# Kernel optimization log

Measured on AMD Instinct MI355X. Metric: run time of the kernel, lower is better.

## Reference

```python
import jax, jax.numpy as jnp
import numpy as np

HEADS = 8
HID = 128
N_A = 10000
N_B = 10000
E = 120000
NG = 8  # graphs in batch
F_A = 256
F_B = 128
NEG_SLOPE = 0.2


def _gat(h_src, h_dst, src, dst, ws, wd, a_s, a_d, bias, num_dst):
    """PyG GATConv, bipartite, concat=False, add_self_loops=False."""
    hs = (h_src @ ws).reshape(-1, HEADS, HID)   # [N_src, H, C]
    hd = (h_dst @ wd).reshape(-1, HEADS, HID)   # [N_dst, H, C]
    al_s = jnp.sum(hs * a_s, axis=-1)           # [N_src, H]
    al_d = jnp.sum(hd * a_d, axis=-1)           # [N_dst, H]
    e = jax.nn.leaky_relu(al_s[src] + al_d[dst], NEG_SLOPE)  # [E, H]
    m = jax.ops.segment_max(e, dst, num_segments=num_dst)
    ex = jnp.exp(e - m[dst])
    denom = jax.ops.segment_sum(ex, dst, num_segments=num_dst)
    alpha = ex / (denom[dst] + 1e-16)           # segment softmax over in-edges
    msg = hs[src] * alpha[:, :, None]           # [E, H, C]
    out = jax.ops.segment_sum(msg, dst, num_segments=num_dst)
    return out.mean(axis=1) + bias              # concat=False -> head mean + bias


def _mean_pool(x, batch, num_graphs):
    s = jax.ops.segment_sum(x, batch, num_segments=num_graphs)
    cnt = jax.ops.segment_sum(jnp.ones((x.shape[0],), x.dtype), batch, num_segments=num_graphs)
    return s / jnp.maximum(cnt, 1.0)[:, None]


def setup_inputs() -> dict:
    key = jax.random.key(0)
    ks = iter(jax.random.split(key, 48))
    rn = lambda shape, s=0.05: jax.random.normal(next(ks), shape, jnp.float32) * s
    inp = {
        'x_a': jax.random.normal(next(ks), (N_A, F_A), jnp.float32),
        'x_b': jax.random.normal(next(ks), (N_B, F_B), jnp.float32),
        'edge_ab': jax.random.randint(next(ks), (2, E), 0, N_A, jnp.int32),
        'edge_ba': jax.random.randint(next(ks), (2, E), 0, N_B, jnp.int32),
        'batch_a': jnp.sort(jax.random.randint(next(ks), (N_A,), 0, NG, jnp.int32)),
        'batch_b': jnp.sort(jax.random.randint(next(ks), (N_B,), 0, NG, jnp.int32)),
        'lin_a_w': rn((F_A, HID)), 'lin_a_b': rn((HID,)),
        'lin_b_w': rn((F_B, HID)), 'lin_b_b': rn((HID,)),
        'fc_w': rn((2 * HID, 1)), 'fc_b': rn((1,)),
    }
    for layer in ('1', '2'):
        for rel in ('ab', 'ba'):
            inp[f'w{layer}s_{rel}'] = rn((HID, HEADS * HID))
            inp[f'w{layer}d_{rel}'] = rn((HID, HEADS * HID))
            inp[f'a{layer}s_{rel}'] = rn((HEADS, HID))
            inp[f'a{layer}d_{rel}'] = rn((HEADS, HID))
            inp[f'b{layer}_{rel}'] = rn((HID,))
    return inp


def reference(x_a, x_b, edge_ab, edge_ba, batch_a, batch_b,
              lin_a_w, lin_a_b, lin_b_w, lin_b_b, fc_w, fc_b,
              w1s_ab, w1d_ab, a1s_ab, a1d_ab, b1_ab,
              w1s_ba, w1d_ba, a1s_ba, a1d_ba, b1_ba,
              w2s_ab, w2d_ab, a2s_ab, a2d_ab, b2_ab,
              w2s_ba, w2d_ba, a2s_ba, a2d_ba, b2_ba):
    ha = jax.nn.relu(x_a @ lin_a_w + lin_a_b)
    hb = jax.nn.relu(x_b @ lin_b_w + lin_b_b)
    # layer 1 (each dst type receives exactly one relation -> HeteroConv mean is identity)
    hb1 = _gat(ha, hb, edge_ab[0], edge_ab[1], w1s_ab, w1d_ab, a1s_ab, a1d_ab, b1_ab, N_B)
    ha1 = _gat(hb, ha, edge_ba[0], edge_ba[1], w1s_ba, w1d_ba, a1s_ba, a1d_ba, b1_ba, N_A)
    ha1 = jax.nn.relu(ha1)
    hb1 = jax.nn.relu(hb1)
    # layer 2
    hb2 = _gat(ha1, hb1, edge_ab[0], edge_ab[1], w2s_ab, w2d_ab, a2s_ab, a2d_ab, b2_ab, N_B)
    ha2 = _gat(hb1, ha1, edge_ba[0], edge_ba[1], w2s_ba, w2d_ba, a2s_ba, a2d_ba, b2_ba, N_A)
    pa = _mean_pool(ha2, batch_a, NG)
    pb = _mean_pool(hb2, batch_b, NG)
    g = jnp.concatenate([pa, pb], axis=1)       # [NG, 2*HID]
    return (g @ fc_w + fc_b).squeeze(-1)        # [NG]
```

## Files before the change

kernel.cpp:

```cpp
#include <hip/hip_runtime.h>
#include <math.h>

#define HID 128
#define HEADS 8

typedef __attribute__((ext_vector_type(8))) short s16x8;
typedef __attribute__((ext_vector_type(4))) float f32x4;

__device__ __forceinline__ unsigned short bf16_rne(float x) {
  unsigned u = __float_as_uint(x);
  unsigned r = u + 0x7FFFu + ((u >> 16) & 1u);
  return (unsigned short)(r >> 16);
}
__device__ __forceinline__ float bf16f(unsigned short h) {
  return __uint_as_float(((unsigned)h) << 16);
}

struct RSeg { float* out; const float* bias; int M; int rowbase; };

__global__ __launch_bounds__(256) void reduce_epi(
    const float* __restrict__ P, int Mtot, int KS, float scale, int do_relu,
    RSeg s0, RSeg s1)
{
  int idx = blockIdx.x * 256 + threadIdx.x;
  if (idx >= Mtot * 32) return;
  int r = idx >> 5;
  int c = (idx & 31) << 2;
  float* outp; const float* bias; int rl;
  if (s1.M > 0 && r >= s1.rowbase) {
    rl = r - s1.rowbase; if (rl >= s1.M) return; outp = s1.out; bias = s1.bias;
  } else {
    rl = r; if (rl >= s0.M) return; outp = s0.out; bias = s0.bias;
  }
  float4 acc = make_float4(0.f, 0.f, 0.f, 0.f);
  for (int z = 0; z < KS; z++) {
    const float4 v = *(const float4*)(P + ((size_t)z * Mtot + r) * HID + c);
    acc.x += v.x; acc.y += v.y; acc.z += v.z; acc.w += v.w;
  }
  const float4 b = *(const float4*)(bias + c);
  acc.x = acc.x * scale + b.x;
  acc.y = acc.y * scale + b.y;
  acc.z = acc.z * scale + b.z;
  acc.w = acc.w * scale + b.w;
  if (do_relu) {
    acc.x = acc.x > 0.f ? acc.x : 0.f;
    acc.y = acc.y > 0.f ? acc.y : 0.f;
    acc.z = acc.z > 0.f ? acc.z : 0.f;
    acc.w = acc.w > 0.f ? acc.w : 0.f;
  }
  *(float4*)(outp + (size_t)rl * HID + c) = acc;
}

struct PrepArgs {
  const float* W[8];
  const float* a[8];
  unsigned short* WThi[4];
  unsigned short* WTlo[4];
  float* v[8];
};

__global__ __launch_bounds__(256) void prep_hist(
    PrepArgs p, const int* __restrict__ dst_ab, const int* __restrict__ dst_ba,
    int* __restrict__ cnt_ab, int* __restrict__ cnt_ba, int E)
{
  int bid = blockIdx.x;
  if (bid < 2048) {
    int g = bid >> 9;
    int idx = ((bid & 511) << 8) + threadIdx.x;
    int kidx = idx & 1023;
    int c = idx >> 10;
    int h = kidx >> 7, k = kidx & 127;
    float wv = p.W[2 * g][(size_t)k * (HEADS * HID) + h * HID + c];
    unsigned short hi = bf16_rne(wv);
    unsigned short lo = bf16_rne(wv - bf16f(hi));
    p.WThi[g][idx] = hi;
    p.WTlo[g][idx] = lo;
  } else if (bid < 2080) {
    int u = bid - 2048;
    int wi = u >> 2;
    int gid = ((u & 3) << 8) + threadIdx.x;
    int k = gid >> 3, h = gid & 7;
    const float* wr = p.W[wi] + (size_t)k * (HEADS * HID) + h * HID;
    const float* ar = p.a[wi] + (size_t)h * HID;
    float s = 0.f;
    for (int c = 0; c < HID; c++) s = fmaf(wr[c], ar[c], s);
    p.v[wi][gid] = s;
  } else {
    int gid = (bid - 2080) * 256 + threadIdx.x;
    if (gid < E) atomicAdd(&cnt_ab[dst_ab[gid]], 1);
    else if (gid < 2 * E) atomicAdd(&cnt_ba[dst_ba[gid - E]], 1);
  }
}

__global__ __launch_bounds__(1024) void scan2(
    const int* __restrict__ cnt_ab, const int* __restrict__ cnt_ba,
    int* __restrict__ ip_ab, int* __restrict__ ip_ba, int n_ab, int n_ba)
{
  const int* cnt = (blockIdx.x == 0) ? cnt_ab : cnt_ba;
  int* indptr = (blockIdx.x == 0) ? ip_ab : ip_ba;
  int n = (blockIdx.x == 0) ? n_ab : n_ba;
  __shared__ int parts[1024];
  const int tid = threadIdx.x;
  const int base = tid * 10;
  int local[10];
  int s = 0;
#pragma unroll
  for (int j = 0; j < 10; j++) {
    int v = (base + j < n) ? cnt[base + j] : 0;
    local[j] = v; s += v;
  }
  parts[tid] = s;
  __syncthreads();
  for (int off = 1; off < 1024; off <<= 1) {
    int v = (tid >= off) ? parts[tid - off] : 0;
    __syncthreads();
    parts[tid] += v;
    __syncthreads();
  }
  int ex = parts[tid] - s;
#pragma unroll
  for (int j = 0; j < 10; j++) {
    if (base + j < n) indptr[base + j] = ex;
    ex += local[j];
  }
  if (tid == 1023) indptr[n] = parts[1023];
}

struct GSeg { const float* A; const float* B; int M; int K; int yb; };

__global__ __launch_bounds__(256, 3) void scatter_gemm_in(
    const int* __restrict__ edge_ab, const int* __restrict__ edge_ba,
    const int* __restrict__ ip_ab, const int* __restrict__ ip_ba,
    int* __restrict__ cur_ab, int* __restrict__ cur_ba,
    int* __restrict__ srcs_ab, int* __restrict__ srcs_ba, int E, int scat_b,
    GSeg s0, GSeg s1, float* __restrict__ P, int Mtot, int KS)
{
  __shared__ float As[16][132];
  __shared__ float Bs[16][132];
  const int bid0 = blockIdx.x;
  if (bid0 < scat_b) {
    int gid = bid0 * 256 + threadIdx.x;
    if (gid < E) {
      int d = edge_ab[E + gid];
      int pos = ip_ab[d] + atomicAdd(&cur_ab[d], 1);
      srcs_ab[pos] = edge_ab[gid];
    } else if (gid < 2 * E) {
      int g = gid - E;
      int d = edge_ba[E + g];
      int pos = ip_ba[d] + atomicAdd(&cur_ba[d], 1);
      srcs_ba[pos] = edge_ba[g];
    }
    return;
  }
  const int gg = bid0 - scat_b;
  const int nxt = s0.yb + s1.yb;
  const int bx = gg % nxt;
  const int by = gg / nxt;

  const int tid = threadIdx.x;
  const float* A; const float* B; int M, K, rowbase, ytile;
  if (bx < s0.yb) {
    A = s0.A; B = s0.B; M = s0.M; K = s0.K; rowbase = 0; ytile = bx;
  } else {
    A = s1.A; B = s1.B; M = s1.M; K = s1.K; rowbase = s0.yb * 128; ytile = bx - s0.yb;
  }
  const int bm = ytile * 128;
  const int kchunk = K / KS;
  const int kbeg = by * kchunk;

  const int am = tid >> 1;
  const int ak = (tid & 1) << 3;
  const int brr = tid >> 4;
  const int bcc = (tid & 15) << 2;
  const int tx = tid & 15, ty = tid >> 4;

  float acc[64];
#pragma unroll
  for (int i = 0; i < 64; i++) acc[i] = 0.f;

  const int gr = bm + am;
  const float* Arow = A + (size_t)gr * K;
  for (int k0 = kbeg; k0 < kbeg + kchunk; k0 += 16) {
    float4 av0 = make_float4(0.f, 0.f, 0.f, 0.f), av1 = av0;
    if (gr < M) {
      av0 = *(const float4*)(Arow + k0 + ak);
      av1 = *(const float4*)(Arow + k0 + ak + 4);
    }
    const float4 bv0 = *(const float4*)(B + (size_t)(k0 + brr) * HID + bcc);
    const float4 bv1 = *(const float4*)(B + (size_t)(k0 + brr) * HID + bcc + 64);
    As[ak + 0][am] = av0.x; As[ak + 1][am] = av0.y;
    As[ak + 2][am] = av0.z; As[ak + 3][am] = av0.w;
    As[ak + 4][am] = av1.x; As[ak + 5][am] = av1.y;
    As[ak + 6][am] = av1.z; As[ak + 7][am] = av1.w;
    *(float4*)&Bs[brr][bcc] = bv0;
    *(float4*)&Bs[brr][bcc + 64] = bv1;
    __syncthreads();
#pragma unroll
    for (int kk = 0; kk < 16; kk++) {
      const float4 a0 = *(const float4*)&As[kk][ty << 3];
      const float4 a1 = *(const float4*)&As[kk][(ty << 3) + 4];
      const float4 b0 = *(const float4*)&Bs[kk][tx << 3];
      const float4 b1 = *(const float4*)&Bs[kk][(tx << 3) + 4];
      const float ar[8] = {a0.x, a0.y, a0.z, a0.w, a1.x, a1.y, a1.z, a1.w};
      const float bq[8] = {b0.x, b0.y, b0.z, b0.w, b1.x, b1.y, b1.z, b1.w};
#pragma unroll
      for (int i = 0; i < 8; i++)
#pragma unroll
        for (int j = 0; j < 8; j++) acc[i * 8 + j] = fmaf(ar[i], bq[j], acc[i * 8 + j]);
    }
    __syncthreads();
  }
  const size_t prow0 = (size_t)by * Mtot + rowbase + bm;
#pragma unroll
  for (int i = 0; i < 8; i++) {
    float* pp = P + (prow0 + (ty << 3) + i) * HID + (tx << 3);
    *(float4*)pp       = make_float4(acc[i * 8 + 0], acc[i * 8 + 1], acc[i * 8 + 2], acc[i * 8 + 3]);
    *(float4*)(pp + 4) = make_float4(acc[i * 8 + 4], acc[i * 8 + 5], acc[i * 8 + 6], acc[i * 8 + 7]);
  }
}

__global__ __launch_bounds__(256) void compute_al4(
    const float* __restrict__ ha, const float* __restrict__ hb,
    const float* __restrict__ v4,
    float* __restrict__ o0, float* __restrict__ o1,
    float* __restrict__ o2, float* __restrict__ o3, int na, int nb)
{
  __shared__ float vsh[4 * HID * HEADS];
  for (int i = threadIdx.x; i < 4 * HID * HEADS; i += 256) vsh[i] = v4[i];
  __syncthreads();
  int gid = blockIdx.x * 256 + threadIdx.x;
  int row = gid >> 3, h = gid & 7;
  const float* hr; float* o; int q, rl;
  if (row < na)                    { q = 0; rl = row;               hr = ha; o = o0; }
  else if (row < na + nb)          { q = 1; rl = row - na;          hr = hb; o = o1; }
  else if (row < na + 2 * nb)      { q = 2; rl = row - na - nb;     hr = hb; o = o2; }
  else if (row < 2 * na + 2 * nb)  { q = 3; rl = row - na - 2 * nb; hr = ha; o = o3; }
  else return;
  hr += (size_t)rl * HID;
  const float* vq = vsh + q * HID * HEADS;
  float s = 0.f;
  for (int k = 0; k < HID; k++) s = fmaf(hr[k], vq[k * HEADS + h], s);
  o[(size_t)rl * HEADS + h] = s;
}

struct GDir {
  const int* indptr; const int* srcs;
  const float* als; const float* ald;
  const float* h;
  unsigned short* zhi; unsigned short* zlo;
};

__global__ __launch_bounds__(256) void gat_edge2(GDir d0, GDir d1, int n0, int ntot)
{
  const int w = threadIdx.x >> 6;
  const int lane = threadIdx.x & 63;
  const int g = blockIdx.x * 4 + w;
  if (g >= ntot) return;
  const bool first = (g < n0);
  const int n = first ? g : g - n0;
  const int* indptr = first ? d0.indptr : d1.indptr;
  const int* srcs   = first ? d0.srcs   : d1.srcs;
  const float* als  = first ? d0.als    : d1.als;
  const float* ald  = first ? d0.ald    : d1.ald;
  const float* hsrc = first ? d0.h      : d1.h;
  unsigned short* zh = (first ? d0.zhi : d1.zhi) + (size_t)n * (HEADS * HID);
  unsigned short* zl = (first ? d0.zlo : d1.zlo) + (size_t)n * (HEADS * HID);

  const int base = indptr[n];
  const int deg = indptr[n + 1] - base;
  if (deg == 0) {
#pragma unroll
    for (int hh = 0; hh < HEADS; hh++) {
      *(unsigned*)(zh + hh * HID + 2 * lane) = 0u;
      *(unsigned*)(zl + hh * HID + 2 * lane) = 0u;
    }
    return;
  }
  const int eh = lane >> 3, h = lane & 7;
  const float aldn = ald[(size_t)n * HEADS + h];
  const int nch = (deg + 7) >> 3;
  const int ncc = nch < 4 ? nch : 4;

  int sc[4];
  float vc[4];
#pragma unroll
  for (int c = 0; c < 4; c++) {
    int e = c * 8 + eh;
    sc[c] = (c < ncc && e < deg) ? srcs[base + e] : -1;
  }
#pragma unroll
  for (int c = 0; c < 4; c++)
    vc[c] = (sc[c] >= 0) ? als[(size_t)sc[c] * HEADS + h] : 0.f;
  float den = 0.f;
#pragma unroll
  for (int c = 0; c < 4; c++) {
    float v = vc[c] + aldn;
    v = v > 0.f ? v : 0.2f * v;
    float ex = (sc[c] >= 0) ? expf(v) : 0.f;
    vc[c] = ex;
    den += ex;
  }
  for (int e0 = 32; e0 < deg; e0 += 8) {
    int e = e0 + eh;
    if (e < deg) {
      int s = srcs[base + e];
      float v = als[(size_t)s * HEADS + h] + aldn;
      v = v > 0.f ? v : 0.2f * v;
      den += expf(v);
    }
  }
  den += __shfl_xor(den, 8);
  den += __shfl_xor(den, 16);
  den += __shfl_xor(den, 32);

  float acc[16];
#pragma unroll
  for (int i = 0; i < 16; i++) acc[i] = 0.f;
#pragma unroll
  for (int c = 0; c < 4; c++) {
    if (c >= ncc) break;
    const int rem = deg - c * 8;
    const int elim = rem < 8 ? rem : 8;
#pragma unroll
    for (int half = 0; half < 2; half++) {
      if (half * 4 >= elim) break;
      int sj[4];
#pragma unroll
      for (int j = 0; j < 4; j++) {
        int s = __shfl(sc[c], (half * 4 + j) * 8);
        sj[j] = s < 0 ? 0 : s;
      }
      float2 hv[4];
#pragma unroll
      for (int j = 0; j < 4; j++)
        hv[j] = *(const float2*)(hsrc + (size_t)sj[j] * HID + 2 * lane);
#pragma unroll
      for (int j = 0; j < 4; j++) {
#pragma unroll
        for (int hh = 0; hh < 8; hh++) {
          float a = __shfl(vc[c], (half * 4 + j) * 8 + hh);
          acc[2 * hh]     = fmaf(a, hv[j].x, acc[2 * hh]);
          acc[2 * hh + 1] = fmaf(a, hv[j].y, acc[2 * hh + 1]);
        }
      }
    }
  }
  for (int e0 = 32; e0 < deg; e0 += 8) {
    int e = e0 + eh;
    int s = (e < deg) ? srcs[base + e] : -1;
    float ex = 0.f;
    if (s >= 0) {
      float v = als[(size_t)s * HEADS + h] + aldn;
      v = v > 0.f ? v : 0.2f * v;
      ex = expf(v);
    }
    int elim = deg - e0; if (elim > 8) elim = 8;
    for (int e8 = 0; e8 < elim; e8++) {
      int ss = __shfl(s, e8 * 8);
      const float2 hvt = *(const float2*)(hsrc + (size_t)ss * HID + 2 * lane);
#pragma unroll
      for (int hh = 0; hh < 8; hh++) {
        float a = __shfl(ex, e8 * 8 + hh);
        acc[2 * hh]     = fmaf(a, hvt.x, acc[2 * hh]);
        acc[2 * hh + 1] = fmaf(a, hvt.y, acc[2 * hh + 1]);
      }
    }
  }
#pragma unroll
  for (int hh = 0; hh < 8; hh++) {
    float dh = __shfl(den, hh);
    float inv = 1.f / (dh + 1e-16f);
    float x0 = acc[2 * hh] * inv;
    float x1 = acc[2 * hh + 1] * inv;
    unsigned short h0 = bf16_rne(x0), h1 = bf16_rne(x1);
    unsigned short l0 = bf16_rne(x0 - bf16f(h0)), l1 = bf16_rne(x1 - bf16f(h1));
    *(unsigned*)(zh + hh * HID + 2 * lane) = (unsigned)h0 | ((unsigned)h1 << 16);
    *(unsigned*)(zl + hh * HID + 2 * lane) = (unsigned)l0 | ((unsigned)l1 << 16);
  }
}

struct MSeg {
  const unsigned short* Ahi; const unsigned short* Alo;
  const unsigned short* Bhi; const unsigned short* Blo;
  float* out; const float* bias; int M; int yb;
};

__global__ __launch_bounds__(512) void gemm_mfma8(MSeg s0, MSeg s1, float scale, int do_relu)
{
  __shared__ __align__(16) unsigned short smem[24576];
  const int tid = threadIdx.x;
  const unsigned short *Ahi, *Alo, *Bhi, *Blo; const float* bias; float* out; int M, ytile;
  if ((int)blockIdx.x < s0.yb) {
    Ahi = s0.Ahi; Alo = s0.Alo; Bhi = s0.Bhi; Blo = s0.Blo;
    out = s0.out; bias = s0.bias; M = s0.M; ytile = blockIdx.x;
  } else {
    Ahi = s1.Ahi; Alo = s1.Alo; Bhi = s1.Bhi; Blo = s1.Blo;
    out = s1.out; bias = s1.bias; M = s1.M; ytile = blockIdx.x - s0.yb;
  }
  const int bm = ytile * 64;
  const int half = tid >> 8;
  const int t = tid & 255;
  const int kbase = half * 512;
  unsigned short* sm = smem + half * 12288;

  const int sr = t >> 2;
  const int sg = t & 3;
  const int g1 = sg ^ ((sr >> 1) & 3);
  const int sr2 = sr + 64;
  const int g2 = sg ^ ((sr2 >> 1) & 3);
  const int aslot  = sr * 32 + g1 * 8;
  const int bslotA = sr * 32 + g1 * 8;
  const int bslotB = sr2 * 32 + g2 * 8;
  const unsigned short* gA  = Ahi + (size_t)(bm + sr) * 1024 + kbase + sg * 8;
  const unsigned short* gAl = Alo + (size_t)(bm + sr) * 1024 + kbase + sg * 8;
  const unsigned short* gB0 = Bhi + (size_t)sr  * 1024 + kbase + sg * 8;
  const unsigned short* gB1 = Bhi + (size_t)sr2 * 1024 + kbase + sg * 8;
  const unsigned short* gC0 = Blo + (size_t)sr  * 1024 + kbase + sg * 8;
  const unsigned short* gC1 = Blo + (size_t)sr2 * 1024 + kbase + sg * 8;

  const int l = t & 63;
  const int w = t >> 6;
  const int kg = l >> 4;
  int aoff[4], boff[2];
#pragma unroll
  for (int mi = 0; mi < 4; mi++) {
    int r = mi * 16 + (l & 15);
    aoff[mi] = r * 32 + (kg ^ ((r >> 1) & 3)) * 8;
  }
#pragma unroll
  for (int ni = 0; ni < 2; ni++) {
    int r = w * 32 + ni * 16 + (l & 15);
    boff[ni] = r * 32 + (kg ^ ((r >> 1) & 3)) * 8;
  }

  f32x4 acc[4][2];
  const f32x4 z4 = {0.f, 0.f, 0.f, 0.f};
#pragma unroll
  for (int mi = 0; mi < 4; mi++)
#pragma unroll
    for (int ni = 0; ni < 2; ni++) acc[mi][ni] = z4;

  uint4 rA  = *(const uint4*)gA;
  uint4 rAl = *(const uint4*)gAl;
  uint4 rB0 = *(const uint4*)gB0;
  uint4 rB1 = *(const uint4*)gB1;
  uint4 rC0 = *(const uint4*)gC0;
  uint4 rC1 = *(const uint4*)gC1;

  for (int ks = 0; ks < 16; ks++) {
    *(uint4*)&sm[aslot]         = rA;
    *(uint4*)&sm[2048 + aslot]  = rAl;
    *(uint4*)&sm[4096 + bslotA] = rB0;
    *(uint4*)&sm[4096 + bslotB] = rB1;
    *(uint4*)&sm[8192 + bslotA] = rC0;
    *(uint4*)&sm[8192 + bslotB] = rC1;
    __syncthreads();
    if (ks < 15) {
      const int k0 = (ks + 1) * 32;
      rA  = *(const uint4*)(gA  + k0);
      rAl = *(const uint4*)(gAl + k0);
      rB0 = *(const uint4*)(gB0 + k0);
      rB1 = *(const uint4*)(gB1 + k0);
      rC0 = *(const uint4*)(gC0 + k0);
      rC1 = *(const uint4*)(gC1 + k0);
    }
    s16x8 bh0 = *(const s16x8*)&sm[4096 + boff[0]];
    s16x8 bh1 = *(const s16x8*)&sm[4096 + boff[1]];
    s16x8 bl0 = *(const s16x8*)&sm[8192 + boff[0]];
    s16x8 bl1 = *(const s16x8*)&sm[8192 + boff[1]];
#pragma unroll
    for (int mi = 0; mi < 4; mi++) {
      s16x8 ah = *(const s16x8*)&sm[aoff[mi]];
      s16x8 al = *(const s16x8*)&sm[2048 + aoff[mi]];
      acc[mi][0] = __builtin_amdgcn_mfma_f32_16x16x32_bf16(ah, bh0, acc[mi][0], 0, 0, 0);
      acc[mi][1] = __builtin_amdgcn_mfma_f32_16x16x32_bf16(ah, bh1, acc[mi][1], 0, 0, 0);
      acc[mi][0] = __builtin_amdgcn_mfma_f32_16x16x32_bf16(ah, bl0, acc[mi][0], 0, 0, 0);
      acc[mi][1] = __builtin_amdgcn_mfma_f32_16x16x32_bf16(ah, bl1, acc[mi][1], 0, 0, 0);
      acc[mi][0] = __builtin_amdgcn_mfma_f32_16x16x32_bf16(al, bh0, acc[mi][0], 0, 0, 0);
      acc[mi][1] = __builtin_amdgcn_mfma_f32_16x16x32_bf16(al, bh1, acc[mi][1], 0, 0, 0);
      acc[mi][0] = __builtin_amdgcn_mfma_f32_16x16x32_bf16(al, bl0, acc[mi][0], 0, 0, 0);
      acc[mi][1] = __builtin_amdgcn_mfma_f32_16x16x32_bf16(al, bl1, acc[mi][1], 0, 0, 0);
    }
    __syncthreads();
  }

  float* fred = (float*)smem;
  const int q = l >> 4, cl = l & 15;
  if (half == 1) {
#pragma unroll
    for (int ni = 0; ni < 2; ni++) {
      const int col = w * 32 + ni * 16 + cl;
#pragma unroll
      for (int mi = 0; mi < 4; mi++) {
        const f32x4 v = acc[mi][ni];
#pragma unroll
        for (int j = 0; j < 4; j++)
          fred[(mi * 16 + q * 4 + j) * 128 + col] = v[j];
      }
    }
  }
  __syncthreads();
  if (half == 0) {
#pragma unroll
    for (int ni = 0; ni < 2; ni++) {
      const int col = w * 32 + ni * 16 + cl;
      const float bv = bias[col];
#pragma unroll
      for (int mi = 0; mi < 4; mi++) {
        const int rt = mi * 16 + q * 4;
        const f32x4 v = acc[mi][ni];
#pragma unroll
        for (int j = 0; j < 4; j++) {
          const int r = bm + rt + j;
          if (r < M) {
            float x = (v[j] + fred[(rt + j) * 128 + col]) * scale + bv;
            if (do_relu) x = fmaxf(x, 0.f);
            out[(size_t)r * HID + col] = x;
          }
        }
      }
    }
  }
}

__global__ __launch_bounds__(256) void pool_fin(
    const float* __restrict__ ha, const float* __restrict__ hb,
    const int* __restrict__ batch_a, const int* __restrict__ batch_b,
    const float* __restrict__ fc_w, const float* __restrict__ fc_b,
    float* __restrict__ gsum, int* __restrict__ ticket,
    float* __restrict__ out, int na, int nb, int ng)
{
  const bool isA = blockIdx.x < 160;
  const float* h = isA ? ha : hb;
  const int* batch = isA ? batch_a : batch_b;
  const float* wseg = isA ? fc_w : fc_w + HID;
  float* gs = isA ? gsum : gsum + 8;
  const int n = isA ? na : nb;
  const int b = isA ? blockIdx.x : blockIdx.x - 160;

  __shared__ float sg[8];
  __shared__ int lastf;
  if (threadIdx.x < 8) sg[threadIdx.x] = 0.f;
  __syncthreads();
  const int lane = threadIdx.x & 63;
  const int wv = threadIdx.x >> 6;
  const int gw = b * 4 + wv;
  const int tw = 160 * 4;
  const float2 w2 = *(const float2*)(wseg + lane * 2);
  for (int r = gw; r < n; r += tw) {
    float2 hv = *(const float2*)(h + (size_t)r * HID + lane * 2);
    float s = hv.x * w2.x + hv.y * w2.y;
#pragma unroll
    for (int off = 32; off > 0; off >>= 1) s += __shfl_down(s, off, 64);
    if (lane == 0) atomicAdd(&sg[batch[r]], s);
  }
  __syncthreads();
  if (threadIdx.x < 8) atomicAdd(&gs[threadIdx.x], sg[threadIdx.x]);
  if (threadIdx.x == 0) {
    __threadfence();
    int tk = atomicAdd(ticket, 1);
    lastf = (tk == (int)gridDim.x - 1);
  }
  __syncthreads();
  if (lastf) {
    int g = threadIdx.x;
    if (g < ng) {
      int l, r, lo;
      l = 0; r = na; while (l < r) { int m = (l + r) >> 1; if (batch_a[m] < g) l = m + 1; else r = m; } lo = l;
      r = na; while (l < r) { int m = (l + r) >> 1; if (batch_a[m] < g + 1) l = m + 1; else r = m; }
      int ca = l - lo; if (ca < 1) ca = 1;
      l = 0; r = nb; while (l < r) { int m = (l + r) >> 1; if (batch_b[m] < g) l = m + 1; else r = m; } lo = l;
      r = nb; while (l < r) { int m = (l + r) >> 1; if (batch_b[m] < g + 1) l = m + 1; else r = m; }
      int cb = l - lo; if (cb < 1) cb = 1;
      float va = atomicAdd(&gsum[g], 0.f);
      float vb = atomicAdd(&gsum[8 + g], 0.f);
      out[g] = va / (float)ca + vb / (float)cb + fc_b[0];
    }
  }
}

extern "C" void kernel_launch(void* const* d_in, const int* in_sizes, int n_in,
                              void* d_out, int out_size, void* d_ws, size_t ws_size,
                              hipStream_t stream)
{
  const float* x_a = (const float*)d_in[0];
  const float* x_b = (const float*)d_in[1];
  const int* edge_ab = (const int*)d_in[2];
  const int* edge_ba = (const int*)d_in[3];
  const int* batch_a = (const int*)d_in[4];
  const int* batch_b = (const int*)d_in[5];
  const float* lin_a_w = (const float*)d_in[6];
  const float* lin_a_b = (const float*)d_in[7];
  const float* lin_b_w = (const float*)d_in[8];
  const float* lin_b_b = (const float*)d_in[9];
  const float* fc_w = (const float*)d_in[10];
  const float* fc_b = (const float*)d_in[11];

  const int NA = in_sizes[4];
  const int NB = in_sizes[5];
  const int E  = in_sizes[2] / 2;
  const int FA = in_sizes[0] / NA;
  const int FB = in_sizes[1] / NB;
  const int NG = out_size;
  const int NMAX = NA > NB ? NA : NB;
  const int NAp = (NA + 127) & ~127, NBp = (NB + 127) & ~127;
  const int NMAXp = NAp > NBp ? NAp : NBp;
  const int yba = NAp / 128, ybb = NBp / 128;
  const int Mtot = NAp + NBp;

  auto al256 = [](size_t b) { return (b + 255) & ~(size_t)255; };
  size_t fixed = 0;
  fixed += 3 * al256((size_t)NAp * HID * 4) + 3 * al256((size_t)NBp * HID * 4);
  fixed += 2 * al256((size_t)NMAXp * 1024 * 2);
  fixed += al256((size_t)8 * 131072 * 2);
  fixed += al256((size_t)8 * HID * HEADS * 4);
  fixed += 2 * al256((size_t)NAp * HEADS * 4) + 2 * al256((size_t)NBp * HEADS * 4);
  fixed += al256(((size_t)4 * NMAX + 24) * 4);
  fixed += al256((size_t)(NB + 1) * 4) + al256((size_t)(NA + 1) * 4);
  fixed += 2 * al256((size_t)E * 4);
  fixed += 8192;
  const size_t zba_sz = 2 * al256((size_t)NAp * 1024 * 2);
  const size_t pslice = al256((size_t)Mtot * HID * 4);

  int KS = 4; bool dual = true;
  if (fixed + zba_sz + 4 * pslice <= ws_size)      { dual = true;  KS = 4; }
  else if (fixed + zba_sz + 2 * pslice <= ws_size) { dual = true;  KS = 2; }
  else if (fixed + 4 * pslice <= ws_size)          { dual = false; KS = 4; }
  else if (fixed + 2 * pslice <= ws_size)          { dual = false; KS = 2; }
  else if (fixed + 1 * pslice <= ws_size)          { dual = false; KS = 1; }
  else return;

  char* w = (char*)d_ws;
  auto carve = [&](size_t bytes) -> void* {
    void* p = (void*)w;
    w += (bytes + 255) & ~(size_t)255;
    return p;
  };
  float* ha0 = (float*)carve((size_t)NAp * HID * 4);
  float* hb0 = (float*)carve((size_t)NBp * HID * 4);
  float* ha1 = (float*)carve((size_t)NAp * HID * 4);
  float* hb1 = (float*)carve((size_t)NBp * HID * 4);
  float* ha2 = (float*)carve((size_t)NAp * HID * 4);
  float* hb2 = (float*)carve((size_t)NBp * HID * 4);
  unsigned short* zab_hi = (unsigned short*)carve((size_t)NMAXp * 1024 * 2);
  unsigned short* zab_lo = (unsigned short*)carve((size_t)NMAXp * 1024 * 2);
  unsigned short* zba_hi = dual ? (unsigned short*)carve((size_t)NAp * 1024 * 2) : zab_hi;
  unsigned short* zba_lo = dual ? (unsigned short*)carve((size_t)NAp * 1024 * 2) : zab_lo;
  float* P   = (float*)carve((size_t)KS * Mtot * HID * 4);
  unsigned short* WT = (unsigned short*)carve((size_t)8 * 131072 * 2);
  float* vv  = (float*)carve((size_t)8 * HID * HEADS * 4);
  float* als_ab = (float*)carve((size_t)NAp * HEADS * 4);
  float* ald_ab = (float*)carve((size_t)NBp * HEADS * 4);
  float* als_ba = (float*)carve((size_t)NBp * HEADS * 4);
  float* ald_ba = (float*)carve((size_t)NAp * HEADS * 4);
  int* csrblk = (int*)carve(((size_t)4 * NMAX + 24) * 4);
  int* indptr_ab = (int*)carve((size_t)(NB + 1) * 4);
  int* indptr_ba = (int*)carve((size_t)(NA + 1) * 4);
  int* srcs_ab   = (int*)carve((size_t)E * 4);
  int* srcs_ba   = (int*)carve((size_t)E * 4);
  if ((size_t)(w - (char*)d_ws) > ws_size) return;

  int* cnt_ab = csrblk;
  int* cnt_ba = csrblk + NMAX;
  int* cur_ab = csrblk + 2 * NMAX;
  int* cur_ba = csrblk + 3 * NMAX;
  float* gsum = (float*)(csrblk + 4 * NMAX);
  int* ticket = csrblk + 4 * NMAX + 16;

  hipMemsetAsync(csrblk, 0, ((size_t)4 * NMAX + 24) * 4, stream);

  PrepArgs pa;
  const int wi_idx[8] = {12, 13, 17, 18, 22, 23, 27, 28};
  const int ai_idx[8] = {14, 15, 19, 20, 24, 25, 29, 30};
  for (int i = 0; i < 8; i++) {
    pa.W[i] = (const float*)d_in[wi_idx[i]];
    pa.a[i] = (const float*)d_in[ai_idx[i]];
    pa.v[i] = vv + (size_t)i * HID * HEADS;
  }
  for (int g = 0; g < 4; g++) {
    pa.WThi[g] = WT + (size_t)g * 131072;
    pa.WTlo[g] = WT + (size_t)(4 + g) * 131072;
  }
  const int hist_b = (2 * E + 255) / 256;
  prep_hist<<<2080 + hist_b, 256, 0, stream>>>(pa, edge_ab + E, edge_ba + E,
                                               cnt_ab, cnt_ba, E);
  scan2<<<2, 1024, 0, stream>>>(cnt_ab, cnt_ba, indptr_ab, indptr_ba, NB, NA);

  {
    GSeg sa = {x_a, lin_a_w, NA, FA, yba};
    GSeg sb = {x_b, lin_b_w, NB, FB, ybb};
    const int scat_b = (2 * E + 255) / 256;
    scatter_gemm_in<<<scat_b + (yba + ybb) * KS, 256, 0, stream>>>(
        edge_ab, edge_ba, indptr_ab, indptr_ba, cur_ab, cur_ba,
        srcs_ab, srcs_ba, E, scat_b, sa, sb, P, Mtot, KS);
    RSeg ra = {ha0, lin_a_b, NA, 0};
    RSeg rb = {hb0, lin_b_b, NB, yba * 128};
    reduce_epi<<<(Mtot * 32 + 255) / 256, 256, 0, stream>>>(P, Mtot, KS, 1.f, 1, ra, rb);
  }

  auto run_layer = [&](int L, const float* haP, const float* hbP,
                       float* haN, float* hbN, const float* b_ab, const float* b_ba,
                       int relu) {
    compute_al4<<<((2 * (NA + NB)) * HEADS + 255) / 256, 256, 0, stream>>>(
        haP, hbP, vv + (size_t)L * 4 * HID * HEADS,
        als_ab, ald_ab, als_ba, ald_ba, NA, NB);
    GDir dab = {indptr_ab, srcs_ab, als_ab, ald_ab, haP, zab_hi, zab_lo};
    GDir dba = {indptr_ba, srcs_ba, als_ba, ald_ba, hbP, zba_hi, zba_lo};
    const int gab = 2 * L, gba = 2 * L + 1;
    MSeg mab = {zab_hi, zab_lo, WT + (size_t)gab * 131072, WT + (size_t)(4 + gab) * 131072,
                hbN, b_ab, NB, NBp / 64};
    MSeg mba = {zba_hi, zba_lo, WT + (size_t)gba * 131072, WT + (size_t)(4 + gba) * 131072,
                haN, b_ba, NA, NAp / 64};
    if (dual) {
      gat_edge2<<<(NB + NA + 3) / 4, 256, 0, stream>>>(dab, dba, NB, NB + NA);
      gemm_mfma8<<<NBp / 64 + NAp / 64, 512, 0, stream>>>(mab, mba, 1.f / HEADS, relu);
    } else {
      MSeg mz = {nullptr, nullptr, nullptr, nullptr, nullptr, nullptr, 0, 0};
      gat_edge2<<<(NB + 3) / 4, 256, 0, stream>>>(dab, dab, NB, NB);
      gemm_mfma8<<<NBp / 64, 512, 0, stream>>>(mab, mz, 1.f / HEADS, relu);
      gat_edge2<<<(NA + 3) / 4, 256, 0, stream>>>(dba, dba, NA, NA);
      gemm_mfma8<<<NAp / 64, 512, 0, stream>>>(mba, mz, 1.f / HEADS, relu);
    }
  };

  run_layer(0, ha0, hb0, ha1, hb1, (const float*)d_in[16], (const float*)d_in[21], 1);
  run_layer(1, ha1, hb1, ha2, hb2, (const float*)d_in[26], (const float*)d_in[31], 0);

  pool_fin<<<320, 256, 0, stream>>>(ha2, hb2, batch_a, batch_b, fc_w, fc_b,
                                    gsum, ticket, (float*)d_out, NA, NB, NG);
}
```

Measured before the change: 391.2 us.

## Replace FP32 split-K input projection with bf16x3 MFMA GEMM and fused epilogue

The input linear layers move from an FP32 SIMT GEMM with split-K partials plus a separate reduce/bias/relu kernel to an MFMA kernel. It emulates fp32 with hi/lo bf16 splits (four MFMAs per product pair). Bias and relu are fused into the epilogue, which removes the partial buffer and the reduce launch. Weights are pre-split in the prep kernel, and edge scattering becomes its own kernel instead of sharing a launch with the GEMM. Accuracy is a bit below true fp32, and the scatter now runs serially before the GEMM instead of alongside it.

```diff
diff --git a/kernel.cpp b/kernel.cpp
--- a/kernel.cpp
+++ b/kernel.cpp
@@ -14,41 +14,6 @@
 }
 __device__ __forceinline__ float bf16f(unsigned short h) {
   return __uint_as_float(((unsigned)h) << 16);
-}
-
-struct RSeg { float* out; const float* bias; int M; int rowbase; };
-
-__global__ __launch_bounds__(256) void reduce_epi(
-    const float* __restrict__ P, int Mtot, int KS, float scale, int do_relu,
-    RSeg s0, RSeg s1)
-{
-  int idx = blockIdx.x * 256 + threadIdx.x;
-  if (idx >= Mtot * 32) return;
-  int r = idx >> 5;
-  int c = (idx & 31) << 2;
-  float* outp; const float* bias; int rl;
-  if (s1.M > 0 && r >= s1.rowbase) {
-    rl = r - s1.rowbase; if (rl >= s1.M) return; outp = s1.out; bias = s1.bias;
-  } else {
-    rl = r; if (rl >= s0.M) return; outp = s0.out; bias = s0.bias;
-  }
-  float4 acc = make_float4(0.f, 0.f, 0.f, 0.f);
-  for (int z = 0; z < KS; z++) {
-    const float4 v = *(const float4*)(P + ((size_t)z * Mtot + r) * HID + c);
-    acc.x += v.x; acc.y += v.y; acc.z += v.z; acc.w += v.w;
-  }
-  const float4 b = *(const float4*)(bias + c);
-  acc.x = acc.x * scale + b.x;
-  acc.y = acc.y * scale + b.y;
-  acc.z = acc.z * scale + b.z;
-  acc.w = acc.w * scale + b.w;
-  if (do_relu) {
-    acc.x = acc.x > 0.f ? acc.x : 0.f;
-    acc.y = acc.y > 0.f ? acc.y : 0.f;
-    acc.z = acc.z > 0.f ? acc.z : 0.f;
-    acc.w = acc.w > 0.f ? acc.w : 0.f;
-  }
-  *(float4*)(outp + (size_t)rl * HID + c) = acc;
 }
 
 struct PrepArgs {
@@ -58,9 +23,15 @@
   unsigned short* WTlo[4];
   float* v[8];
 };
+struct PrepX {
+  const float* lwa; const float* lwb;
+  unsigned short *wa_hi, *wa_lo, *wb_hi, *wb_lo;
+  int KA, KB, nwa, nwb;
+};
 
 __global__ __launch_bounds__(256) void prep_hist(
-    PrepArgs p, const int* __restrict__ dst_ab, const int* __restrict__ dst_ba,
+    PrepArgs p, PrepX px,
+    const int* __restrict__ dst_ab, const int* __restrict__ dst_ba,
     int* __restrict__ cnt_ab, int* __restrict__ cnt_ba, int E)
 {
   int bid = blockIdx.x;
@@ -85,8 +56,28 @@
     float s = 0.f;
     for (int c = 0; c < HID; c++) s = fmaf(wr[c], ar[c], s);
     p.v[wi][gid] = s;
+  } else if (bid < 2080 + px.nwa) {
+    int idx = (bid - 2080) * 256 + threadIdx.x;
+    if (idx < px.KA * HID) {
+      int k = idx % px.KA, c = idx / px.KA;
+      float wv = px.lwa[(size_t)k * HID + c];
+      unsigned short hi = bf16_rne(wv);
+      unsigned short lo = bf16_rne(wv - bf16f(hi));
+      px.wa_hi[idx] = hi;
+      px.wa_lo[idx] = lo;
+    }
+  } else if (bid < 2080 + px.nwa + px.nwb) {
+    int idx = (bid - 2080 - px.nwa) * 256 + threadIdx.x;
+    if (idx < px.KB * HID) {
+      int k = idx % px.KB, c = idx / px.KB;
+      float wv = px.lwb[(size_t)k * HID + c];
+      unsigned short hi = bf16_rne(wv);
+      unsigned short lo = bf16_rne(wv - bf16f(hi));
+      px.wb_hi[idx] = hi;
+      px.wb_lo[idx] = lo;
+    }
   } else {
-    int gid = (bid - 2080) * 256 + threadIdx.x;
+    int gid = (bid - 2080 - px.nwa - px.nwb) * 256 + threadIdx.x;
     if (gid < E) atomicAdd(&cnt_ab[dst_ab[gid]], 1);
     else if (gid < 2 * E) atomicAdd(&cnt_ba[dst_ba[gid - E]], 1);
   }
@@ -126,96 +117,163 @@
   if (tid == 1023) indptr[n] = parts[1023];
 }
 
-struct GSeg { const float* A; const float* B; int M; int K; int yb; };
-
-__global__ __launch_bounds__(256, 3) void scatter_gemm_in(
+__global__ __launch_bounds__(256) void scatter2(
     const int* __restrict__ edge_ab, const int* __restrict__ edge_ba,
     const int* __restrict__ ip_ab, const int* __restrict__ ip_ba,
     int* __restrict__ cur_ab, int* __restrict__ cur_ba,
-    int* __restrict__ srcs_ab, int* __restrict__ srcs_ba, int E, int scat_b,
-    GSeg s0, GSeg s1, float* __restrict__ P, int Mtot, int KS)
-{
-  __shared__ float As[16][132];
-  __shared__ float Bs[16][132];
-  const int bid0 = blockIdx.x;
-  if (bid0 < scat_b) {
-    int gid = bid0 * 256 + threadIdx.x;
-    if (gid < E) {
-      int d = edge_ab[E + gid];
-      int pos = ip_ab[d] + atomicAdd(&cur_ab[d], 1);
-      srcs_ab[pos] = edge_ab[gid];
-    } else if (gid < 2 * E) {
-      int g = gid - E;
-      int d = edge_ba[E + g];
-      int pos = ip_ba[d] + atomicAdd(&cur_ba[d], 1);
-      srcs_ba[pos] = edge_ba[g];
-    }
-    return;
-  }
-  const int gg = bid0 - scat_b;
-  const int nxt = s0.yb + s1.yb;
-  const int bx = gg % nxt;
-  const int by = gg / nxt;
-
+    int* __restrict__ srcs_ab, int* __restrict__ srcs_ba, int E)
+{
+  int gid = blockIdx.x * 256 + threadIdx.x;
+  if (gid < E) {
+    int d = edge_ab[E + gid];
+    int pos = ip_ab[d] + atomicAdd(&cur_ab[d], 1);
+    srcs_ab[pos] = edge_ab[gid];
+  } else if (gid < 2 * E) {
+    int g = gid - E;
+    int d = edge_ba[E + g];
+    int pos = ip_ba[d] + atomicAdd(&cur_ba[d], 1);
+    srcs_ba[pos] = edge_ba[g];
+  }
+}
+
+struct ISeg {
+  const float* A;
+  const unsigned short* Bhi; const unsigned short* Blo;
+  float* out; const float* bias; int M; int K; int yb;
+};
+
+__global__ __launch_bounds__(256) void gemm_mfma_in(ISeg s0, ISeg s1)
+{
+  __shared__ __align__(16) unsigned short smem[12288];
   const int tid = threadIdx.x;
-  const float* A; const float* B; int M, K, rowbase, ytile;
-  if (bx < s0.yb) {
-    A = s0.A; B = s0.B; M = s0.M; K = s0.K; rowbase = 0; ytile = bx;
+  const float* A; const unsigned short *Bhi, *Blo; const float* bias; float* out;
+  int M, K, ytile;
+  if ((int)blockIdx.x < s0.yb) {
+    A = s0.A; Bhi = s0.Bhi; Blo = s0.Blo; out = s0.out; bias = s0.bias;
+    M = s0.M; K = s0.K; ytile = blockIdx.x;
   } else {
-    A = s1.A; B = s1.B; M = s1.M; K = s1.K; rowbase = s0.yb * 128; ytile = bx - s0.yb;
-  }
-  const int bm = ytile * 128;
-  const int kchunk = K / KS;
-  const int kbeg = by * kchunk;
-
-  const int am = tid >> 1;
-  const int ak = (tid & 1) << 3;
-  const int brr = tid >> 4;
-  const int bcc = (tid & 15) << 2;
-  const int tx = tid & 15, ty = tid >> 4;
-
-  float acc[64];
-#pragma unroll
-  for (int i = 0; i < 64; i++) acc[i] = 0.f;
-
-  const int gr = bm + am;
-  const float* Arow = A + (size_t)gr * K;
-  for (int k0 = kbeg; k0 < kbeg + kchunk; k0 += 16) {
-    float4 av0 = make_float4(0.f, 0.f, 0.f, 0.f), av1 = av0;
-    if (gr < M) {
-      av0 = *(const float4*)(Arow + k0 + ak);
-      av1 = *(const float4*)(Arow + k0 + ak + 4);
-    }
-    const float4 bv0 = *(const float4*)(B + (size_t)(k0 + brr) * HID + bcc);
-    const float4 bv1 = *(const float4*)(B + (size_t)(k0 + brr) * HID + bcc + 64);
-    As[ak + 0][am] = av0.x; As[ak + 1][am] = av0.y;
-    As[ak + 2][am] = av0.z; As[ak + 3][am] = av0.w;
-    As[ak + 4][am] = av1.x; As[ak + 5][am] = av1.y;
-    As[ak + 6][am] = av1.z; As[ak + 7][am] = av1.w;
-    *(float4*)&Bs[brr][bcc] = bv0;
-    *(float4*)&Bs[brr][bcc + 64] = bv1;
+    A = s1.A; Bhi = s1.Bhi; Blo = s1.Blo; out = s1.out; bias = s1.bias;
+    M = s1.M; K = s1.K; ytile = blockIdx.x - s0.yb;
+  }
+  const int bm = ytile * 64;
+  const int nks = K >> 5;
+
+  const int sr = tid >> 2;
+  const int sg = tid & 3;
+  const int g1 = sg ^ ((sr >> 1) & 3);
+  const int sr2 = sr + 64;
+  const int g2 = sg ^ ((sr2 >> 1) & 3);
+  const int aslot  = sr * 32 + g1 * 8;
+  const int bslotA = sr * 32 + g1 * 8;
+  const int bslotB = sr2 * 32 + g2 * 8;
+  const int gr = bm + sr;
+  const bool arow_ok = (gr < M);
+  const float* gA = A + (size_t)gr * K + sg * 8;
+  const unsigned short* gB0 = Bhi + (size_t)sr  * K + sg * 8;
+  const unsigned short* gB1 = Bhi + (size_t)sr2 * K + sg * 8;
+  const unsigned short* gC0 = Blo + (size_t)sr  * K + sg * 8;
+  const unsigned short* gC1 = Blo + (size_t)sr2 * K + sg * 8;
+
+  const int l = tid & 63;
+  const int w = tid >> 6;
+  const int kg = l >> 4;
+  int aoff[4], boff[2];
+#pragma unroll
+  for (int mi = 0; mi < 4; mi++) {
+    int r = mi * 16 + (l & 15);
+    aoff[mi] = r * 32 + (kg ^ ((r >> 1) & 3)) * 8;
+  }
+#pragma unroll
+  for (int ni = 0; ni < 2; ni++) {
+    int r = w * 32 + ni * 16 + (l & 15);
+    boff[ni] = r * 32 + (kg ^ ((r >> 1) & 3)) * 8;
+  }
+
+  f32x4 acc[4][2];
+  const f32x4 z4 = {0.f, 0.f, 0.f, 0.f};
+#pragma unroll
+  for (int mi = 0; mi < 4; mi++)
+#pragma unroll
+    for (int ni = 0; ni < 2; ni++) acc[mi][ni] = z4;
+
+  float4 fa0 = make_float4(0.f, 0.f, 0.f, 0.f), fa1 = fa0;
+  if (arow_ok) { fa0 = *(const float4*)gA; fa1 = *(const float4*)(gA + 4); }
+  uint4 rB0 = *(const uint4*)gB0;
+  uint4 rB1 = *(const uint4*)gB1;
+  uint4 rC0 = *(const uint4*)gC0;
+  uint4 rC1 = *(const uint4*)gC1;
+
+  for (int ks = 0; ks < nks; ks++) {
+    {
+      const float f[8] = {fa0.x, fa0.y, fa0.z, fa0.w, fa1.x, fa1.y, fa1.z, fa1.w};
+      unsigned au[4], lu[4];
+#pragma unroll
+      for (int i = 0; i < 4; i++) {
+        unsigned short h0 = bf16_rne(f[2 * i]);
+        unsigned short l0 = bf16_rne(f[2 * i] - bf16f(h0));
+        unsigned short h1 = bf16_rne(f[2 * i + 1]);
+        unsigned short l1 = bf16_rne(f[2 * i + 1] - bf16f(h1));
+        au[i] = (unsigned)h0 | ((unsigned)h1 << 16);
+        lu[i] = (unsigned)l0 | ((unsigned)l1 << 16);
+      }
+      *(uint4*)&smem[aslot]        = make_uint4(au[0], au[1], au[2], au[3]);
+      *(uint4*)&smem[2048 + aslot] = make_uint4(lu[0], lu[1], lu[2], lu[3]);
+    }
+    *(uint4*)&smem[4096 + bslotA] = rB0;
+    *(uint4*)&smem[4096 + bslotB] = rB1;
+    *(uint4*)&smem[8192 + bslotA] = rC0;
+    *(uint4*)&smem[8192 + bslotB] = rC1;
     __syncthreads();
-#pragma unroll
-    for (int kk = 0; kk < 16; kk++) {
-      const float4 a0 = *(const float4*)&As[kk][ty << 3];
-      const float4 a1 = *(const float4*)&As[kk][(ty << 3) + 4];
-      const float4 b0 = *(const float4*)&Bs[kk][tx << 3];
-      const float4 b1 = *(const float4*)&Bs[kk][(tx << 3) + 4];
-      const float ar[8] = {a0.x, a0.y, a0.z, a0.w, a1.x, a1.y, a1.z, a1.w};
-      const float bq[8] = {b0.x, b0.y, b0.z, b0.w, b1.x, b1.y, b1.z, b1.w};
-#pragma unroll
-      for (int i = 0; i < 8; i++)
-#pragma unroll
-        for (int j = 0; j < 8; j++) acc[i * 8 + j] = fmaf(ar[i], bq[j], acc[i * 8 + j]);
+    if (ks < nks - 1) {
+      const int k0 = (ks + 1) * 32;
+      if (arow_ok) {
+        fa0 = *(const float4*)(gA + k0);
+        fa1 = *(const float4*)(gA + k0 + 4);
+      }
+      rB0 = *(const uint4*)(gB0 + k0);
+      rB1 = *(const uint4*)(gB1 + k0);
+      rC0 = *(const uint4*)(gC0 + k0);
+      rC1 = *(const uint4*)(gC1 + k0);
+    }
+    s16x8 bh0 = *(const s16x8*)&smem[4096 + boff[0]];
+    s16x8 bh1 = *(const s16x8*)&smem[4096 + boff[1]];
+    s16x8 bl0 = *(const s16x8*)&smem[8192 + boff[0]];
+    s16x8 bl1 = *(const s16x8*)&smem[8192 + boff[1]];
+#pragma unroll
+    for (int mi = 0; mi < 4; mi++) {
+      s16x8 ah = *(const s16x8*)&smem[aoff[mi]];
+      s16x8 al = *(const s16x8*)&smem[2048 + aoff[mi]];
+      acc[mi][0] = __builtin_amdgcn_mfma_f32_16x16x32_bf16(ah, bh0, acc[mi][0], 0, 0, 0);
+      acc[mi][1] = __builtin_amdgcn_mfma_f32_16x16x32_bf16(ah, bh1, acc[mi][1], 0, 0, 0);
+      acc[mi][0] = __builtin_amdgcn_mfma_f32_16x16x32_bf16(ah, bl0, acc[mi][0], 0, 0, 0);
+      acc[mi][1] = __builtin_amdgcn_mfma_f32_16x16x32_bf16(ah, bl1, acc[mi][1], 0, 0, 0);
+      acc[mi][0] = __builtin_amdgcn_mfma_f32_16x16x32_bf16(al, bh0, acc[mi][0], 0, 0, 0);
+      acc[mi][1] = __builtin_amdgcn_mfma_f32_16x16x32_bf16(al, bh1, acc[mi][1], 0, 0, 0);
+      acc[mi][0] = __builtin_amdgcn_mfma_f32_16x16x32_bf16(al, bl0, acc[mi][0], 0, 0, 0);
+      acc[mi][1] = __builtin_amdgcn_mfma_f32_16x16x32_bf16(al, bl1, acc[mi][1], 0, 0, 0);
     }
     __syncthreads();
   }
-  const size_t prow0 = (size_t)by * Mtot + rowbase + bm;
-#pragma unroll
-  for (int i = 0; i < 8; i++) {
-    float* pp = P + (prow0 + (ty << 3) + i) * HID + (tx << 3);
-    *(float4*)pp       = make_float4(acc[i * 8 + 0], acc[i * 8 + 1], acc[i * 8 + 2], acc[i * 8 + 3]);
-    *(float4*)(pp + 4) = make_float4(acc[i * 8 + 4], acc[i * 8 + 5], acc[i * 8 + 6], acc[i * 8 + 7]);
+
+  const int q = l >> 4, cl = l & 15;
+#pragma unroll
+  for (int ni = 0; ni < 2; ni++) {
+    const int col = w * 32 + ni * 16 + cl;
+    const float bv = bias[col];
+#pragma unroll
+    for (int mi = 0; mi < 4; mi++) {
+      const int r0 = bm + mi * 16 + q * 4;
+      const f32x4 v = acc[mi][ni];
+#pragma unroll
+      for (int j = 0; j < 4; j++) {
+        const int r = r0 + j;
+        if (r < M) {
+          float x = v[j] + bv;
+          x = fmaxf(x, 0.f);
+          out[(size_t)r * HID + col] = x;
+        }
+      }
+    }
   }
 }
 
@@ -605,14 +663,13 @@
   const int NMAX = NA > NB ? NA : NB;
   const int NAp = (NA + 127) & ~127, NBp = (NB + 127) & ~127;
   const int NMAXp = NAp > NBp ? NAp : NBp;
-  const int yba = NAp / 128, ybb = NBp / 128;
-  const int Mtot = NAp + NBp;
 
   auto al256 = [](size_t b) { return (b + 255) & ~(size_t)255; };
   size_t fixed = 0;
   fixed += 3 * al256((size_t)NAp * HID * 4) + 3 * al256((size_t)NBp * HID * 4);
   fixed += 2 * al256((size_t)NMAXp * 1024 * 2);
   fixed += al256((size_t)8 * 131072 * 2);
+  fixed += 2 * al256((size_t)FA * HID * 2) + 2 * al256((size_t)FB * HID * 2);
   fixed += al256((size_t)8 * HID * HEADS * 4);
   fixed += 2 * al256((size_t)NAp * HEADS * 4) + 2 * al256((size_t)NBp * HEADS * 4);
   fixed += al256(((size_t)4 * NMAX + 24) * 4);
@@ -620,15 +677,9 @@
   fixed += 2 * al256((size_t)E * 4);
   fixed += 8192;
   const size_t zba_sz = 2 * al256((size_t)NAp * 1024 * 2);
-  const size_t pslice = al256((size_t)Mtot * HID * 4);
-
-  int KS = 4; bool dual = true;
-  if (fixed + zba_sz + 4 * pslice <= ws_size)      { dual = true;  KS = 4; }
-  else if (fixed + zba_sz + 2 * pslice <= ws_size) { dual = true;  KS = 2; }
-  else if (fixed + 4 * pslice <= ws_size)          { dual = false; KS = 4; }
-  else if (fixed + 2 * pslice <= ws_size)          { dual = false; KS = 2; }
-  else if (fixed + 1 * pslice <= ws_size)          { dual = false; KS = 1; }
-  else return;
+
+  bool dual = (fixed + zba_sz <= ws_size);
+  if (fixed > ws_size) return;
 
   char* w = (char*)d_ws;
   auto carve = [&](size_t bytes) -> void* {
@@ -646,8 +697,11 @@
   unsigned short* zab_lo = (unsigned short*)carve((size_t)NMAXp * 1024 * 2);
   unsigned short* zba_hi = dual ? (unsigned short*)carve((size_t)NAp * 1024 * 2) : zab_hi;
   unsigned short* zba_lo = dual ? (unsigned short*)carve((size_t)NAp * 1024 * 2) : zab_lo;
-  float* P   = (float*)carve((size_t)KS * Mtot * HID * 4);
   unsigned short* WT = (unsigned short*)carve((size_t)8 * 131072 * 2);
+  unsigned short* wa_hi = (unsigned short*)carve((size_t)FA * HID * 2);
+  unsigned short* wa_lo = (unsigned short*)carve((size_t)FA * HID * 2);
+  unsigned short* wb_hi = (unsigned short*)carve((size_t)FB * HID * 2);
+  unsigned short* wb_lo = (unsigned short*)carve((size_t)FB * HID * 2);
   float* vv  = (float*)carve((size_t)8 * HID * HEADS * 4);
   float* als_ab = (float*)carve((size_t)NAp * HEADS * 4);
   float* ald_ab = (float*)carve((size_t)NBp * HEADS * 4);
@@ -681,21 +735,23 @@
     pa.WThi[g] = WT + (size_t)g * 131072;
     pa.WTlo[g] = WT + (size_t)(4 + g) * 131072;
   }
+  PrepX px;
+  px.lwa = lin_a_w; px.lwb = lin_b_w;
+  px.wa_hi = wa_hi; px.wa_lo = wa_lo; px.wb_hi = wb_hi; px.wb_lo = wb_lo;
+  px.KA = FA; px.KB = FB;
+  px.nwa = (FA * HID + 255) / 256;
+  px.nwb = (FB * HID + 255) / 256;
   const int hist_b = (2 * E + 255) / 256;
-  prep_hist<<<2080 + hist_b, 256, 0, stream>>>(pa, edge_ab + E, edge_ba + E,
-                                               cnt_ab, cnt_ba, E);
+  prep_hist<<<2080 + px.nwa + px.nwb + hist_b, 256, 0, stream>>>(
+      pa, px, edge_ab + E, edge_ba + E, cnt_ab, cnt_ba, E);
   scan2<<<2, 1024, 0, stream>>>(cnt_ab, cnt_ba, indptr_ab, indptr_ba, NB, NA);
+  scatter2<<<(2 * E + 255) / 256, 256, 0, stream>>>(
+      edge_ab, edge_ba, indptr_ab, indptr_ba, cur_ab, cur_ba, srcs_ab, srcs_ba, E);
 
   {
-    GSeg sa = {x_a, lin_a_w, NA, FA, yba};
-    GSeg sb = {x_b, lin_b_w, NB, FB, ybb};
-    const int scat_b = (2 * E + 255) / 256;
-    scatter_gemm_in<<<scat_b + (yba + ybb) * KS, 256, 0, stream>>>(
-        edge_ab, edge_ba, indptr_ab, indptr_ba, cur_ab, cur_ba,
-        srcs_ab, srcs_ba, E, scat_b, sa, sb, P, Mtot, KS);
-    RSeg ra = {ha0, lin_a_b, NA, 0};
-    RSeg rb = {hb0, lin_b_b, NB, yba * 128};
-    reduce_epi<<<(Mtot * 32 + 255) / 256, 256, 0, stream>>>(P, Mtot, KS, 1.f, 1, ra, rb);
+    ISeg sa = {x_a, wa_hi, wa_lo, ha0, lin_a_b, NA, FA, NAp / 64};
+    ISeg sb = {x_b, wb_hi, wb_lo, hb0, lin_b_b, NB, FB, NBp / 64};
+    gemm_mfma_in<<<NAp / 64 + NBp / 64, 256, 0, stream>>>(sa, sb);
   }
 
   auto run_layer = [&](int L, const float* haP, const float* hbP,
```

Result: faster. 371.9 us (-4.9%).
